# Kernel tuning notes

Measured on AMD Instinct MI355X. Metric: run time of the kernel, lower is better.

The kernel has to match this reference:

```python
import jax, jax.numpy as jnp
import numpy as np

H = 1024   # hidden size
NH = 16    # num attention heads
HD = H // NH  # head dim = 64


def setup_inputs() -> dict:
    key = jax.random.key(0)
    ks = jax.random.split(key, 8)
    B, S = 2, 2048
    scale = 0.02
    return {
        "hidden_states": jax.random.normal(ks[0], (B, S, H), dtype=jnp.float32),
        "attention_mask": jnp.zeros((B, 1, 1, S), dtype=jnp.float32),
        "Wq": jax.random.normal(ks[1], (H, H), dtype=jnp.float32) * scale,
        "bq": jnp.zeros((H,), dtype=jnp.float32),
        "Wk": jax.random.normal(ks[2], (H, H), dtype=jnp.float32) * scale,
        "bk": jnp.zeros((H,), dtype=jnp.float32),
        "Wv": jax.random.normal(ks[3], (H, H), dtype=jnp.float32) * scale,
        "bv": jnp.zeros((H,), dtype=jnp.float32),
    }


def reference(hidden_states, attention_mask, Wq, bq, Wk, bk, Wv, bv):
    B, S, _ = hidden_states.shape

    def split_heads(x):  # [B,S,H] -> [B,NH,S,HD]
        return x.reshape(B, S, NH, HD).transpose(0, 2, 1, 3)

    q = split_heads(hidden_states @ Wq.T + bq)
    k = split_heads(hidden_states @ Wk.T + bk)
    v = split_heads(hidden_states @ Wv.T + bv)

    # raw attention scores [B,NH,S,S]
    scores = jnp.einsum("bhqd,bhkd->bhqk", q, k) / jnp.sqrt(jnp.float32(HD))
    scores = scores + attention_mask  # additive mask, broadcast [B,1,1,S]
    probs = jax.nn.softmax(scores, axis=-1)
    # dropout(p=0.1) is identity in eval mode

    ctx = jnp.einsum("bhqk,bhkd->bhqd", probs, v)  # [B,NH,S,HD]
    return ctx.transpose(0, 2, 1, 3).reshape(B, S, H)
```

## Files before the change

### kernel.cpp

```cpp
#include <hip/hip_runtime.h>
#include <hip/hip_bf16.h>
#include <math.h>

#define HSZ 1024
#define NHD 16
#define SEQ 2048
#define BSZ 2
#define MTOT (BSZ*SEQ)

typedef __attribute__((ext_vector_type(4)))  float  f32x4;
typedef __attribute__((ext_vector_type(8)))  __bf16 bf16x8;

#define LOG2E 1.4426950408889634f

#if __has_builtin(__builtin_amdgcn_exp2f)
#define EXP2(x) __builtin_amdgcn_exp2f(x)
#else
#define EXP2(x) exp2f(x)
#endif

__device__ __forceinline__ unsigned short f2bf(float x) {
    union { float f; unsigned u; } v; v.f = x;
    unsigned r = v.u + 0x7FFFu + ((v.u >> 16) & 1u);
    return (unsigned short)(r >> 16);
}
__device__ __forceinline__ float bf2f(unsigned short u) {
    union { unsigned u; float f; } v; v.u = ((unsigned)u) << 16; return v.f;
}
__device__ __forceinline__ unsigned cvtpk(float lo, float hi) {
    unsigned r;
    asm("v_cvt_pk_bf16_f32 %0, %1, %2" : "=v"(r) : "v"(lo), "v"(hi));
    return r;
}

__global__ __launch_bounds__(256) void cvt_all(
    const float* __restrict__ h,  unsigned short* __restrict__ hd,
    const float* __restrict__ w0, unsigned short* __restrict__ w0d,
    const float* __restrict__ w1, unsigned short* __restrict__ w1d,
    const float* __restrict__ w2, unsigned short* __restrict__ w2d,
    const float* __restrict__ mask, unsigned short* __restrict__ mexpb)
{
    const int bid = blockIdx.x;
    if (bid >= 3584) {
        const int o = ((bid - 3584) * 256 + threadIdx.x) * 8;
        float4 a = *(const float4*)(mask + o);
        float4 b = *(const float4*)(mask + o + 4);
        uint4 v;
        v.x = f2bf(EXP2(a.x * LOG2E)) | ((unsigned)f2bf(EXP2(a.y * LOG2E)) << 16);
        v.y = f2bf(EXP2(a.z * LOG2E)) | ((unsigned)f2bf(EXP2(a.w * LOG2E)) << 16);
        v.z = f2bf(EXP2(b.x * LOG2E)) | ((unsigned)f2bf(EXP2(b.y * LOG2E)) << 16);
        v.w = f2bf(EXP2(b.z * LOG2E)) | ((unsigned)f2bf(EXP2(b.w * LOG2E)) << 16);
        *(uint4*)(mexpb + o) = v;
        return;
    }
    const float* s; unsigned short* d; int i;
    if (bid < 2048)      { s = h;  d = hd;  i = bid; }
    else if (bid < 2560) { s = w0; d = w0d; i = bid - 2048; }
    else if (bid < 3072) { s = w1; d = w1d; i = bid - 2560; }
    else                 { s = w2; d = w2d; i = bid - 3072; }
    const int o = (i * 256 + threadIdx.x) * 8;
    float4 a = *(const float4*)(s + o);
    float4 b = *(const float4*)(s + o + 4);
    uint4 v;
    v.x = f2bf(a.x) | ((unsigned)f2bf(a.y) << 16);
    v.y = f2bf(a.z) | ((unsigned)f2bf(a.w) << 16);
    v.z = f2bf(b.x) | ((unsigned)f2bf(b.y) << 16);
    v.w = f2bf(b.z) | ((unsigned)f2bf(b.w) << 16);
    *(uint4*)(d + o) = v;
}

__global__ __launch_bounds__(256) void qkv_gemm(
    const unsigned short* __restrict__ hb,
    const unsigned short* __restrict__ wq,
    const unsigned short* __restrict__ wk,
    const unsigned short* __restrict__ wv,
    const float* __restrict__ bq, const float* __restrict__ bk,
    const float* __restrict__ bv, const unsigned short* __restrict__ mexpb,
    unsigned short* __restrict__ qo, char* __restrict__ ko,
    char* __restrict__ vo)
{
    __shared__ __align__(16) unsigned short As[64 * 32];
    __shared__ __align__(16) unsigned short Bs[128 * 32];

    const int t = threadIdx.x;
    const int w = t >> 6, l = t & 63, g = l >> 4, c = l & 15;
    const int lin  = blockIdx.y * 24 + blockIdx.x;
    const int nlin = (lin & 7) * 192 + (lin >> 3);
    const int bn = nlin % 24, bm = nlin / 24;
    const int which = bn >> 3;
    const int n0 = (bn & 7) << 7;
    const int m0 = bm << 6;
    const unsigned short* W = (which == 0) ? wq : (which == 1) ? wk : wv;
    const float* bb = (which == 0) ? bq : (which == 1) ? bk : bv;
    const float scale = (which == 0) ? 0.125f * LOG2E : 1.0f;
    const int wr = w >> 1, wc = w & 1;

    float mexpf[8];
    if (which == 2) {
        #pragma unroll
        for (int mi = 0; mi < 2; ++mi) {
            const int mrow = m0 + wr * 32 + mi * 16 + g * 4;
            const int bi = mrow >> 11, si = mrow & 2047;
            uint2 mv = *(const uint2*)(mexpb + bi * SEQ + si);
            mexpf[mi * 4 + 0] = bf2f((unsigned short)(mv.x & 0xFFFF));
            mexpf[mi * 4 + 1] = bf2f((unsigned short)(mv.x >> 16));
            mexpf[mi * 4 + 2] = bf2f((unsigned short)(mv.y & 0xFFFF));
            mexpf[mi * 4 + 3] = bf2f((unsigned short)(mv.y >> 16));
        }
    }

    f32x4 acc[2][4];
    #pragma unroll
    for (int mi = 0; mi < 2; ++mi)
        #pragma unroll
        for (int ni = 0; ni < 4; ++ni) acc[mi][ni] = {0.f, 0.f, 0.f, 0.f};

    const int srow = l >> 2;
    const int sgr  = l & 3;

    for (int k0 = 0; k0 < HSZ; k0 += 32) {
        {
            const int row = (w << 4) + srow;
            const int sg = sgr ^ ((row >> 1) & 3);
            const char* ga = (const char*)hb +
                (((size_t)(m0 + row) << 10) + k0) * 2 + sg * 16;
            __builtin_amdgcn_global_load_lds(
                (const __attribute__((address_space(1))) unsigned*)ga,
                (__attribute__((address_space(3))) unsigned*)((char*)As + w * 1024),
                16, 0, 0);
        }
        #pragma unroll
        for (int i2 = 0; i2 < 2; ++i2) {
            const int chunk = w + i2 * 4;
            const int row = (chunk << 4) + srow;
            const int sg = sgr ^ ((row >> 1) & 3);
            const char* gb = (const char*)W +
                (((size_t)(n0 + row) << 10) + k0) * 2 + sg * 16;
            __builtin_amdgcn_global_load_lds(
                (const __attribute__((address_space(1))) unsigned*)gb,
                (__attribute__((address_space(3))) unsigned*)((char*)Bs + chunk * 1024),
                16, 0, 0);
        }
        __syncthreads();

        bf16x8 af[2], bfr[4];
        #pragma unroll
        for (int mi = 0; mi < 2; ++mi) {
            const int row = wr * 32 + mi * 16 + c;
            const int gg = g ^ ((row >> 1) & 3);
            af[mi] = *(const bf16x8*)((const char*)As + row * 64 + gg * 16);
        }
        #pragma unroll
        for (int ni = 0; ni < 4; ++ni) {
            const int row = wc * 64 + ni * 16 + c;
            const int gg = g ^ ((row >> 1) & 3);
            bfr[ni] = *(const bf16x8*)((const char*)Bs + row * 64 + gg * 16);
        }
        __builtin_amdgcn_s_setprio(1);
        #pragma unroll
        for (int mi = 0; mi < 2; ++mi)
            #pragma unroll
            for (int ni = 0; ni < 4; ++ni)
                acc[mi][ni] = __builtin_amdgcn_mfma_f32_16x16x32_bf16(
                    af[mi], bfr[ni], acc[mi][ni], 0, 0, 0);
        __builtin_amdgcn_s_setprio(0);
        __syncthreads();
    }

    #pragma unroll
    for (int ni = 0; ni < 4; ++ni) {
        const int ncol = n0 + wc * 64 + ni * 16 + c;
        const int hh = ncol >> 6, d = ncol & 63;
        const float bsc = bb[ncol] * scale;
        #pragma unroll
        for (int mi = 0; mi < 2; ++mi) {
            #pragma unroll
            for (int j = 0; j < 4; ++j) {
                const int mrow = m0 + wr * 32 + mi * 16 + g * 4 + j;
                const int bi = mrow >> 11, si = mrow & 2047;
                float vf = acc[mi][ni][j] * scale + bsc;
                if (which == 2) vf *= mexpf[mi * 4 + j];
                const unsigned short val = f2bf(vf);
                const size_t bhoff = (size_t)(bi * NHD + hh);
                if (which == 0) {
                    qo[((bhoff * SEQ + si) << 6) + d] = val;
                } else if (which == 1) {
                    char* p = ko + (bhoff << 18) + ((size_t)(si >> 6) << 13)
                            + ((si & 63) << 7) + (((d << 1)) ^ ((si & 7) << 4));
                    *(unsigned short*)p = val;
                } else {
                    char* p = vo + (bhoff << 18) + ((size_t)(si >> 6) << 13)
                            + (d << 7) + (((si & 63) << 1) ^ ((d & 7) << 4));
                    *(unsigned short*)p = val;
                }
            }
        }
    }
}

__global__ __launch_bounds__(256) void attn_mfma(
    const unsigned short* __restrict__ qb, const char* __restrict__ kb,
    const char* __restrict__ vb, const unsigned short* __restrict__ mexpb,
    float* __restrict__ out)
{
    __shared__ __align__(16) char Kt[2][8192];
    __shared__ __align__(16) char Vt[2][8192];
    __shared__ __align__(16) unsigned Pl[4][16][32];

    const int t = threadIdx.x;
    const int w = t >> 6, l = t & 63, g = l >> 4, c = l & 15;
    const int qt = blockIdx.x, h = blockIdx.y, b = blockIdx.z;
    const int bh = b * NHD + h;
    const int q0 = qt * 128 + w * 32;

    const unsigned short* qp = qb + ((size_t)bh * SEQ + q0) * 64;
    const char* kbase = kb + ((size_t)bh << 18);
    const char* vbase = vb + ((size_t)bh << 18);
    const unsigned short* mep = mexpb + b * SEQ;

    bf16x8 qf[2][2];
    #pragma unroll
    for (int qh = 0; qh < 2; ++qh)
        #pragma unroll
        for (int p = 0; p < 2; ++p)
            qf[qh][p] = *(const bf16x8*)(qp + (qh * 16 + c) * 64 + p * 32 + g * 8);

    f32x4 o0[4], o1[4];
    #pragma unroll
    for (int tt = 0; tt < 4; ++tt) { o0[tt] = {0.f,0.f,0.f,0.f}; o1[tt] = {0.f,0.f,0.f,0.f}; }
    f32x4 ls0 = {0.f,0.f,0.f,0.f}, ls1 = {0.f,0.f,0.f,0.f};

    auto STAGE = [&](int tile, int buf) {
        const char* kg = kbase + tile * 8192 + w * 2048 + l * 16;
        const char* vg = vbase + tile * 8192 + w * 2048 + l * 16;
        #pragma unroll
        for (int i = 0; i < 2; ++i) {
            __builtin_amdgcn_global_load_lds(
                (const __attribute__((address_space(1))) unsigned*)(kg + i * 1024),
                (__attribute__((address_space(3))) unsigned*)(&Kt[buf][w * 2048 + i * 1024]),
                16, 0, 0);
            __builtin_amdgcn_global_load_lds(
                (const __attribute__((address_space(1))) unsigned*)(vg + i * 1024),
                (__attribute__((address_space(3))) unsigned*)(&Vt[buf][w * 2048 + i * 1024]),
                16, 0, 0);
        }
    };

    STAGE(0, 0);

    int cur = 0;
    for (int kt = 0; kt < 32; ++kt) {
        const int kv0 = kt * 64;

        asm volatile("s_waitcnt vmcnt(0)" ::: "memory");
        __builtin_amdgcn_s_barrier();
        __builtin_amdgcn_sched_barrier(0);

        if (kt < 31) STAGE(kt + 1, cur ^ 1);

        bf16x8 mf[2];
        #pragma unroll
        for (int blk = 0; blk < 2; ++blk)
            mf[blk] = *(const bf16x8*)(mep + kv0 + blk * 32 + g * 8);

        f32x4 s0[4], s1[4];
        #pragma unroll
        for (int t2 = 0; t2 < 4; ++t2) { s0[t2] = {0.f,0.f,0.f,0.f}; s1[t2] = {0.f,0.f,0.f,0.f}; }
        __builtin_amdgcn_s_setprio(1);
        #pragma unroll
        for (int t2 = 0; t2 < 4; ++t2) {
            const bf16x8 k0 = *(const bf16x8*)(&Kt[cur][(t2 * 16 + c) * 128
                                 + ((g * 16) ^ ((c & 7) << 4))]);
            const bf16x8 k1 = *(const bf16x8*)(&Kt[cur][(t2 * 16 + c) * 128
                                 + ((64 + g * 16) ^ ((c & 7) << 4))]);
            s0[t2] = __builtin_amdgcn_mfma_f32_16x16x32_bf16(k0, qf[0][0], s0[t2], 0, 0, 0);
            s0[t2] = __builtin_amdgcn_mfma_f32_16x16x32_bf16(k1, qf[0][1], s0[t2], 0, 0, 0);
            s1[t2] = __builtin_amdgcn_mfma_f32_16x16x32_bf16(k0, qf[1][0], s1[t2], 0, 0, 0);
            s1[t2] = __builtin_amdgcn_mfma_f32_16x16x32_bf16(k1, qf[1][1], s1[t2], 0, 0, 0);
        }
        __builtin_amdgcn_s_setprio(0);

        bf16x8 vfr[4][2];
        #pragma unroll
        for (int tt = 0; tt < 4; ++tt)
            #pragma unroll
            for (int blk = 0; blk < 2; ++blk)
                vfr[tt][blk] = *(const bf16x8*)(&Vt[cur][(tt * 16 + c) * 128
                                     + ((blk * 64 + g * 16) ^ ((c & 7) << 4))]);

        #pragma unroll
        for (int t2 = 0; t2 < 4; ++t2) {
            s0[t2][0] = EXP2(s0[t2][0]); s0[t2][1] = EXP2(s0[t2][1]);
            s0[t2][2] = EXP2(s0[t2][2]); s0[t2][3] = EXP2(s0[t2][3]);
        }
        #pragma unroll
        for (int t2 = 0; t2 < 4; ++t2) {
            uint2 pr;
            pr.x = cvtpk(s0[t2][0], s0[t2][1]);
            pr.y = cvtpk(s0[t2][2], s0[t2][3]);
            *(uint2*)&Pl[w][c][(8 * t2 + 2 * g) ^ ((c & 7) << 2)] = pr;
        }
        {
            bf16x8 pfr[2];
            #pragma unroll
            for (int blk = 0; blk < 2; ++blk)
                pfr[blk] = *(const bf16x8*)&Pl[w][c][(16 * blk + 4 * g) ^ ((c & 7) << 2)];
            __builtin_amdgcn_s_setprio(1);
            #pragma unroll
            for (int blk = 0; blk < 2; ++blk)
                ls0 = __builtin_amdgcn_mfma_f32_16x16x32_bf16(mf[blk], pfr[blk], ls0, 0, 0, 0);
            #pragma unroll
            for (int tt = 0; tt < 4; ++tt)
                #pragma unroll
                for (int blk = 0; blk < 2; ++blk)
                    o0[tt] = __builtin_amdgcn_mfma_f32_16x16x32_bf16(vfr[tt][blk], pfr[blk], o0[tt], 0, 0, 0);
            __builtin_amdgcn_s_setprio(0);
        }

        #pragma unroll
        for (int t2 = 0; t2 < 4; ++t2) {
            s1[t2][0] = EXP2(s1[t2][0]); s1[t2][1] = EXP2(s1[t2][1]);
            s1[t2][2] = EXP2(s1[t2][2]); s1[t2][3] = EXP2(s1[t2][3]);
        }
        #pragma unroll
        for (int t2 = 0; t2 < 4; ++t2) {
            uint2 pr;
            pr.x = cvtpk(s1[t2][0], s1[t2][1]);
            pr.y = cvtpk(s1[t2][2], s1[t2][3]);
            *(uint2*)&Pl[w][c][(8 * t2 + 2 * g) ^ ((c & 7) << 2)] = pr;
        }
        {
            bf16x8 pfr[2];
            #pragma unroll
            for (int blk = 0; blk < 2; ++blk)
                pfr[blk] = *(const bf16x8*)&Pl[w][c][(16 * blk + 4 * g) ^ ((c & 7) << 2)];
            __builtin_amdgcn_s_setprio(1);
            #pragma unroll
            for (int blk = 0; blk < 2; ++blk)
                ls1 = __builtin_amdgcn_mfma_f32_16x16x32_bf16(mf[blk], pfr[blk], ls1, 0, 0, 0);
            #pragma unroll
            for (int tt = 0; tt < 4; ++tt)
                #pragma unroll
                for (int blk = 0; blk < 2; ++blk)
                    o1[tt] = __builtin_amdgcn_mfma_f32_16x16x32_bf16(vfr[tt][blk], pfr[blk], o1[tt], 0, 0, 0);
            __builtin_amdgcn_s_setprio(0);
        }

        cur ^= 1;
    }

    const float li0 = 1.f / ls0[0];
    const float li1 = 1.f / ls1[0];
    #pragma unroll
    for (int tt = 0; tt < 4; ++tt) {
        const size_t r0 = ((size_t)(b * SEQ + q0 + c) << 10) + h * 64 + 16 * tt + 4 * g;
        out[r0 + 0] = o0[tt][0] * li0;
        out[r0 + 1] = o0[tt][1] * li0;
        out[r0 + 2] = o0[tt][2] * li0;
        out[r0 + 3] = o0[tt][3] * li0;
        const size_t r1 = ((size_t)(b * SEQ + q0 + 16 + c) << 10) + h * 64 + 16 * tt + 4 * g;
        out[r1 + 0] = o1[tt][0] * li1;
        out[r1 + 1] = o1[tt][1] * li1;
        out[r1 + 2] = o1[tt][2] * li1;
        out[r1 + 3] = o1[tt][3] * li1;
    }
}

extern "C" void kernel_launch(void* const* d_in, const int* in_sizes, int n_in,
                              void* d_out, int out_size, void* d_ws, size_t ws_size,
                              hipStream_t stream) {
    const float* hid  = (const float*)d_in[0];
    const float* mask = (const float*)d_in[1];
    const float* Wq   = (const float*)d_in[2];
    const float* bq   = (const float*)d_in[3];
    const float* Wk   = (const float*)d_in[4];
    const float* bk   = (const float*)d_in[5];
    const float* Wv   = (const float*)d_in[6];
    const float* bv   = (const float*)d_in[7];
    float* out = (float*)d_out;

    char* ws = (char*)d_ws;
    unsigned short* qbf = (unsigned short*)(ws);
    char*           kbf = ws + 8388608;
    char*           vbf = ws + 16777216;
    unsigned short* hbf = (unsigned short*)(ws + 25165824);
    unsigned short* wqb = (unsigned short*)(ws + 33554432);
    unsigned short* wkb = (unsigned short*)(ws + 35651584);
    unsigned short* wvb = (unsigned short*)(ws + 37748736);
    unsigned short* mxb = (unsigned short*)(ws + 39845888);

    cvt_all<<<3586, 256, 0, stream>>>(hid, hbf, Wq, wqb, Wk, wkb, Wv, wvb,
                                      mask, mxb);
    qkv_gemm<<<dim3(24, 64), 256, 0, stream>>>(hbf, wqb, wkb, wvb,
                                               bq, bk, bv, mxb, qbf, kbf, vbf);
    attn_mfma<<<dim3(16, NHD, BSZ), 256, 0, stream>>>(qbf, kbf, vbf, mxb, out);
}
```

Baseline: 115.4 us.

## Permute K row mapping so P stays in registers, dropping LDS round trip

Reorders which K rows each lane loads, with a matching new XOR swizzle in the projection kernel's K layout, so the QK^T MFMA output already sits in the register order the PV MFMA needs as its B operand. This removes the per-tile write of probabilities to shared memory and the read back, along with the Pl buffer. It couples the K layout written by the projection kernel to the attention kernel's fragment mapping and may change LDS bank-conflict behaviour for K reads.

Measured after the change: 110.9 us. 1.04x faster.

```diff
diff --git a/kernel.cpp b/kernel.cpp
--- a/kernel.cpp
+++ b/kernel.cpp
@@ -185,8 +185,9 @@
                 if (which == 0) {
                     qo[((bhoff * SEQ + si) << 6) + d] = val;
                 } else if (which == 1) {
+                    const int kswz = ((si & 3) | (((si >> 3) & 1) << 2)) << 4;
                     char* p = ko + (bhoff << 18) + ((size_t)(si >> 6) << 13)
-                            + ((si & 63) << 7) + (((d << 1)) ^ ((si & 7) << 4));
+                            + ((si & 63) << 7) + ((d << 1) ^ kswz);
                     *(unsigned short*)p = val;
                 } else {
                     char* p = vo + (bhoff << 18) + ((size_t)(si >> 6) << 13)
@@ -205,7 +206,6 @@
 {
     __shared__ __align__(16) char Kt[2][8192];
     __shared__ __align__(16) char Vt[2][8192];
-    __shared__ __align__(16) unsigned Pl[4][16][32];
 
     const int t = threadIdx.x;
     const int w = t >> 6, l = t & 63, g = l >> 4, c = l & 15;
@@ -248,6 +248,10 @@
 
     STAGE(0, 0);
 
+    const int a_  = c >> 2, bb_ = c & 3;
+    const int kswz = (bb_ | ((a_ & 1) << 2)) << 4;
+    const int krow0 = (8 * a_ + bb_) * 128;
+
     int cur = 0;
     for (int kt = 0; kt < 32; ++kt) {
         const int kv0 = kt * 64;
@@ -263,20 +267,26 @@
         for (int blk = 0; blk < 2; ++blk)
             mf[blk] = *(const bf16x8*)(mep + kv0 + blk * 32 + g * 8);
 
+        bf16x8 kfr[4][2];
+        #pragma unroll
+        for (int tt = 0; tt < 4; ++tt) {
+            const int roff = krow0 + ((tt & 1) * 4 + (tt >> 1) * 32) * 128;
+            #pragma unroll
+            for (int p = 0; p < 2; ++p)
+                kfr[tt][p] = *(const bf16x8*)(&Kt[cur][roff
+                                 + ((p * 64 + g * 16) ^ kswz)]);
+        }
+
         f32x4 s0[4], s1[4];
         #pragma unroll
         for (int t2 = 0; t2 < 4; ++t2) { s0[t2] = {0.f,0.f,0.f,0.f}; s1[t2] = {0.f,0.f,0.f,0.f}; }
         __builtin_amdgcn_s_setprio(1);
         #pragma unroll
         for (int t2 = 0; t2 < 4; ++t2) {
-            const bf16x8 k0 = *(const bf16x8*)(&Kt[cur][(t2 * 16 + c) * 128
-                                 + ((g * 16) ^ ((c & 7) << 4))]);
-            const bf16x8 k1 = *(const bf16x8*)(&Kt[cur][(t2 * 16 + c) * 128
-                                 + ((64 + g * 16) ^ ((c & 7) << 4))]);
-            s0[t2] = __builtin_amdgcn_mfma_f32_16x16x32_bf16(k0, qf[0][0], s0[t2], 0, 0, 0);
-            s0[t2] = __builtin_amdgcn_mfma_f32_16x16x32_bf16(k1, qf[0][1], s0[t2], 0, 0, 0);
-            s1[t2] = __builtin_amdgcn_mfma_f32_16x16x32_bf16(k0, qf[1][0], s1[t2], 0, 0, 0);
-            s1[t2] = __builtin_amdgcn_mfma_f32_16x16x32_bf16(k1, qf[1][1], s1[t2], 0, 0, 0);
+            s0[t2] = __builtin_amdgcn_mfma_f32_16x16x32_bf16(kfr[t2][0], qf[0][0], s0[t2], 0, 0, 0);
+            s0[t2] = __builtin_amdgcn_mfma_f32_16x16x32_bf16(kfr[t2][1], qf[0][1], s0[t2], 0, 0, 0);
+            s1[t2] = __builtin_amdgcn_mfma_f32_16x16x32_bf16(kfr[t2][0], qf[1][0], s1[t2], 0, 0, 0);
+            s1[t2] = __builtin_amdgcn_mfma_f32_16x16x32_bf16(kfr[t2][1], qf[1][1], s1[t2], 0, 0, 0);
         }
         __builtin_amdgcn_s_setprio(0);
 
@@ -293,18 +303,17 @@
             s0[t2][0] = EXP2(s0[t2][0]); s0[t2][1] = EXP2(s0[t2][1]);
             s0[t2][2] = EXP2(s0[t2][2]); s0[t2][3] = EXP2(s0[t2][3]);
         }
-        #pragma unroll
-        for (int t2 = 0; t2 < 4; ++t2) {
-            uint2 pr;
-            pr.x = cvtpk(s0[t2][0], s0[t2][1]);
-            pr.y = cvtpk(s0[t2][2], s0[t2][3]);
-            *(uint2*)&Pl[w][c][(8 * t2 + 2 * g) ^ ((c & 7) << 2)] = pr;
-        }
         {
             bf16x8 pfr[2];
             #pragma unroll
-            for (int blk = 0; blk < 2; ++blk)
-                pfr[blk] = *(const bf16x8*)&Pl[w][c][(16 * blk + 4 * g) ^ ((c & 7) << 2)];
+            for (int blk = 0; blk < 2; ++blk) {
+                uint4 tmp;
+                tmp.x = cvtpk(s0[2*blk][0],   s0[2*blk][1]);
+                tmp.y = cvtpk(s0[2*blk][2],   s0[2*blk][3]);
+                tmp.z = cvtpk(s0[2*blk+1][0], s0[2*blk+1][1]);
+                tmp.w = cvtpk(s0[2*blk+1][2], s0[2*blk+1][3]);
+                pfr[blk] = *(bf16x8*)&tmp;
+            }
             __builtin_amdgcn_s_setprio(1);
             #pragma unroll
             for (int blk = 0; blk < 2; ++blk)
@@ -322,18 +331,17 @@
             s1[t2][0] = EXP2(s1[t2][0]); s1[t2][1] = EXP2(s1[t2][1]);
             s1[t2][2] = EXP2(s1[t2][2]); s1[t2][3] = EXP2(s1[t2][3]);
         }
-        #pragma unroll
-        for (int t2 = 0; t2 < 4; ++t2) {
-            uint2 pr;
-            pr.x = cvtpk(s1[t2][0], s1[t2][1]);
-            pr.y = cvtpk(s1[t2][2], s1[t2][3]);
-            *(uint2*)&Pl[w][c][(8 * t2 + 2 * g) ^ ((c & 7) << 2)] = pr;
-        }
         {
             bf16x8 pfr[2];
             #pragma unroll
-            for (int blk = 0; blk < 2; ++blk)
-                pfr[blk] = *(const bf16x8*)&Pl[w][c][(16 * blk + 4 * g) ^ ((c & 7) << 2)];
+            for (int blk = 0; blk < 2; ++blk) {
+                uint4 tmp;
+                tmp.x = cvtpk(s1[2*blk][0],   s1[2*blk][1]);
+                tmp.y = cvtpk(s1[2*blk][2],   s1[2*blk][3]);
+                tmp.z = cvtpk(s1[2*blk+1][0], s1[2*blk+1][1]);
+                tmp.w = cvtpk(s1[2*blk+1][2], s1[2*blk+1][3]);
+                pfr[blk] = *(bf16x8*)&tmp;
+            }
             __builtin_amdgcn_s_setprio(1);
             #pragma unroll
             for (int blk = 0; blk < 2; ++blk)
```
